# Optimization experiments

Hardware: AMD Instinct MI355X
Metric: run time of the kernel (lower is better)

The kernel has to match this reference:

```python
import jax, jax.numpy as jnp
import numpy as np

T, IN, BATCH = 512, 512, 256
HID, WID = 1024, 512


def setup_inputs() -> dict:
    key = jax.random.key(0)
    k_x, k_wh, k_bh, k_wy, k_by, k_h0 = jax.random.split(key, 6)
    s_h = 1.0 / np.sqrt(HID + IN)  # stabilise sigmoid pre-activations
    s_y = 1.0 / np.sqrt(HID)
    return {
        "xs": jax.random.normal(k_x, (T, IN, BATCH), dtype=jnp.float32),
        "W_h": jax.random.normal(k_wh, (HID, HID + IN), dtype=jnp.float32) * s_h,
        "b_h": jax.random.normal(k_bh, (HID, 1), dtype=jnp.float32) * 0.1,
        "W_y": jax.random.normal(k_wy, (WID, HID), dtype=jnp.float32) * s_y,
        "b_y": jax.random.normal(k_by, (WID, 1), dtype=jnp.float32) * 0.1,
        "h0": jax.random.normal(k_h0, (HID, 1), dtype=jnp.float32),
    }


def reference(xs, W_h, b_h, W_y, b_y, h0):
    # xs: [T, input_size, batch]; returns ys: [T, width, batch]
    batch = xs.shape[2]
    h_init = jnp.tile(h0, (1, batch))  # [HID, batch]

    def step(h, x):
        z = jnp.concatenate([h, x], axis=0)          # [HID+IN, batch]
        h_new = jax.nn.sigmoid(W_h @ z + b_h)        # [HID, batch]
        y = jax.nn.sigmoid(W_y @ h_new + b_y)        # [WID, batch]
        return h_new, y

    _, ys = jax.lax.scan(step, h_init, xs)
    return ys
```

## Files before the change

kernel.cpp:

```cpp
#include <hip/hip_runtime.h>
#include <hip/hip_bf16.h>

#define T_STEPS 512
#define INP     512
#define NB      256
#define HID     1024
#define WID     512
#define KZ      1536
#define ZSZ     (NB * KZ)

typedef short          bf16x8   __attribute__((ext_vector_type(8)));
typedef float          f32x4    __attribute__((ext_vector_type(4)));
typedef float          f32x2    __attribute__((ext_vector_type(2)));
typedef unsigned short ushort8  __attribute__((ext_vector_type(8)));
typedef unsigned short ushort2v __attribute__((ext_vector_type(2)));
typedef unsigned short ushort4v __attribute__((ext_vector_type(4)));
typedef unsigned long long u64;

__device__ __forceinline__ unsigned short f2bf(float x) {
  __hip_bfloat16 h = __float2bfloat16(x);
  return __builtin_bit_cast(unsigned short, h);
}
__device__ __forceinline__ float sigm(float x) { return 1.0f / (1.0f + __expf(-x)); }

#define ZLOAD(dst, p) \
  asm volatile("global_load_dwordx4 %0, %1, off sc0 sc1" : "=v"(dst) : "v"(p))
#define ZWAIT() do { \
  asm volatile("s_waitcnt vmcnt(0)" ::: "memory"); \
  __builtin_amdgcn_sched_barrier(0); \
} while (0)

__device__ __forceinline__ void zst4(unsigned short* p, ushort2v v) {
  __hip_atomic_store((unsigned*)p, __builtin_bit_cast(unsigned, v),
                     __ATOMIC_RELAXED, __HIP_MEMORY_SCOPE_AGENT);
}
__device__ __forceinline__ void zst8(unsigned short* p, ushort4v v) {
  __hip_atomic_store((u64*)p, __builtin_bit_cast(u64, v),
                     __ATOMIC_RELAXED, __HIP_MEMORY_SCOPE_AGENT);
}

__device__ __forceinline__ void poll1(unsigned* p, unsigned tgt) {
  while (__hip_atomic_load(p, __ATOMIC_RELAXED, __HIP_MEMORY_SCOPE_AGENT) < tgt)
    __builtin_amdgcn_s_sleep(1);
}
__device__ __forceinline__ void poll2(u64* p, unsigned lo, unsigned hi) {
  for (;;) {
    const u64 v = __hip_atomic_load(p, __ATOMIC_RELAXED, __HIP_MEMORY_SCOPE_AGENT);
    if ((unsigned)v >= lo && (unsigned)(v >> 32) >= hi) return;
    __builtin_amdgcn_s_sleep(1);
  }
}
__device__ __forceinline__ void arrive(unsigned* ctr) {
  asm volatile("s_waitcnt vmcnt(0)" ::: "memory");
  __syncthreads();
  if (threadIdx.x == 0)
    __hip_atomic_fetch_add(ctr, 1u, __ATOMIC_RELAXED, __HIP_MEMORY_SCOPE_AGENT);
}

__global__ void elman_setup(const float* __restrict__ h0, const float* __restrict__ xs,
                            unsigned short* __restrict__ zT, unsigned* __restrict__ bars) {
  const int b = blockIdx.x;
  if (b == 0) {
    for (int j = threadIdx.x; j < 512; j += blockDim.x) bars[j] = 0u;
  }
  for (int k = threadIdx.x; k < KZ; k += blockDim.x) {
    const float v = (k < HID) ? h0[k] : xs[(size_t)(k - HID) * NB + b];
    zT[(size_t)b * KZ + k] = f2bf(v);
  }
  for (int i = threadIdx.x; i < INP; i += blockDim.x)
    zT[(size_t)ZSZ + (size_t)b * KZ + HID + i] = f2bf(xs[(size_t)(INP + i) * NB + b]);
}

#define PSTR 36
#define PWSZ (32 * PSTR)

__global__ void __launch_bounds__(512, 2) elman_seq(
    const float* __restrict__ xs,
    const float* __restrict__ Wh, const float* __restrict__ bh,
    const float* __restrict__ Wy, const float* __restrict__ by,
    unsigned short* __restrict__ zT, float* __restrict__ out,
    unsigned* __restrict__ bars) {
  __shared__ float P[8 * PWSZ];
  const int wg = blockIdx.x, tid = threadIdx.x;
  const int w = tid >> 6, lane = tid & 63;
  const int lr = lane & 15, lk = lane >> 4;
  unsigned* bar = bars + (wg & 7) * 64;

  if (wg < 128) {
    const int m0 = (wg >> 3) * 64;
    const int n0 = (wg & 7) * 32;
    const int kw = w * 192;
    bf16x8 A[4][6];
#pragma unroll
    for (int mt = 0; mt < 4; ++mt)
#pragma unroll
      for (int kc = 0; kc < 6; ++kc) {
        const float* wp = Wh + (size_t)(m0 + mt * 16 + lr) * KZ + kw + kc * 32 + lk * 8;
        const f32x4 f0 = *(const f32x4*)wp;
        const f32x4 f1 = *(const f32x4*)(wp + 4);
        ushort8 a;
#pragma unroll
        for (int e = 0; e < 4; ++e) { a[e] = f2bf(f0[e]); a[4 + e] = f2bf(f1[e]); }
        A[mt][kc] = __builtin_bit_cast(bf16x8, a);
      }
    const int lcol = tid >> 4;
    const int r2 = (tid & 15) * 2;
    f32x2 bias[2];
#pragma unroll
    for (int hf = 0; hf < 2; ++hf) bias[hf] = *(const f32x2*)&bh[m0 + hf * 32 + r2];
    float* Pw = P + w * PWSZ;

    for (int t = 0; t <= T_STEPS; ++t) {
      if (t < T_STEPS) {
        const unsigned short* zc = zT + (size_t)(t & 3) * ZSZ;
        unsigned short* zn = zT + (size_t)((t + 1) & 3) * ZSZ;
        if (t >= 1) {
          if (tid == 0) poll2((u64*)bar, 16u * (unsigned)t,
                              (t >= 2) ? 8u * (unsigned)(t - 1) : 0u);
          __syncthreads();
        }
        const unsigned short* zb = zc + (size_t)(n0 + lr) * KZ + kw + lk * 8;
        bf16x8 bfr[6][2];
#pragma unroll
        for (int kc = 0; kc < 6; ++kc)
#pragma unroll
          for (int nt = 0; nt < 2; ++nt)
            ZLOAD(bfr[kc][nt], zb + nt * (16 * KZ) + kc * 32);
        ZWAIT();
        f32x4 acc[4][2];
#pragma unroll
        for (int mt = 0; mt < 4; ++mt)
#pragma unroll
          for (int nt = 0; nt < 2; ++nt) acc[mt][nt] = (f32x4){0.f, 0.f, 0.f, 0.f};
#pragma unroll
        for (int kc = 0; kc < 6; ++kc)
#pragma unroll
          for (int nt = 0; nt < 2; ++nt)
#pragma unroll
            for (int mt = 0; mt < 4; ++mt)
              acc[mt][nt] = __builtin_amdgcn_mfma_f32_16x16x32_bf16(A[mt][kc], bfr[kc][nt], acc[mt][nt], 0, 0, 0);
        if (t >= 3 && tid == 0) poll1(bar + 2, 8u * (unsigned)(t - 2));
        __syncthreads();
#pragma unroll
        for (int hf = 0; hf < 2; ++hf) {
#pragma unroll
          for (int mp = 0; mp < 2; ++mp) {
            const int mt = hf * 2 + mp;
#pragma unroll
            for (int nt = 0; nt < 2; ++nt)
              *(f32x4*)&Pw[(nt * 16 + lr) * PSTR + mp * 16 + lk * 4] = acc[mt][nt];
          }
          __syncthreads();
          f32x2 s = {0.f, 0.f};
#pragma unroll
          for (int ww = 0; ww < 8; ++ww)
            s += *(const f32x2*)&P[ww * PWSZ + lcol * PSTR + r2];
          s += bias[hf];
          ushort2v o2;
          o2[0] = f2bf(sigm(s[0]));
          o2[1] = f2bf(sigm(s[1]));
          zst4(zn + (size_t)(n0 + lcol) * KZ + m0 + hf * 32 + r2, o2);
          if (hf == 0) __syncthreads();
        }
      }
      arrive(bar + 0);
    }

  } else if (wg < 192) {
    const int idx = wg - 128;
    const int m0 = (idx >> 3) * 64;
    const int n0 = (idx & 7) * 32;
    const int kw = w * 128;
    bf16x8 A[4][4];
#pragma unroll
    for (int mt = 0; mt < 4; ++mt)
#pragma unroll
      for (int kc = 0; kc < 4; ++kc) {
        const float* wp = Wy + (size_t)(m0 + mt * 16 + lr) * HID + kw + kc * 32 + lk * 8;
        const f32x4 f0 = *(const f32x4*)wp;
        const f32x4 f1 = *(const f32x4*)(wp + 4);
        ushort8 a;
#pragma unroll
        for (int e = 0; e < 4; ++e) { a[e] = f2bf(f0[e]); a[4 + e] = f2bf(f1[e]); }
        A[mt][kc] = __builtin_bit_cast(bf16x8, a);
      }
    const int lcol = tid & 31;
    const int r2 = (tid >> 5) * 2;
    f32x2 bias[2];
#pragma unroll
    for (int hf = 0; hf < 2; ++hf) bias[hf] = *(const f32x2*)&by[m0 + hf * 32 + r2];
    float* Pw = P + w * PWSZ;

    for (int t = 0; t <= T_STEPS; ++t) {
      if (t >= 1) {
        const unsigned short* zc = zT + (size_t)(t & 3) * ZSZ;
        if (tid == 0) poll1(bar + 0, 16u * (unsigned)t);
        __syncthreads();
        const unsigned short* zb = zc + (size_t)(n0 + lr) * KZ + kw + lk * 8;
        bf16x8 bfr[4][2];
#pragma unroll
        for (int kc = 0; kc < 4; ++kc)
#pragma unroll
          for (int nt = 0; nt < 2; ++nt)
            ZLOAD(bfr[kc][nt], zb + nt * (16 * KZ) + kc * 32);
        ZWAIT();
        f32x4 acc[4][2];
#pragma unroll
        for (int mt = 0; mt < 4; ++mt)
#pragma unroll
          for (int nt = 0; nt < 2; ++nt) acc[mt][nt] = (f32x4){0.f, 0.f, 0.f, 0.f};
#pragma unroll
        for (int kc = 0; kc < 4; ++kc)
#pragma unroll
          for (int nt = 0; nt < 2; ++nt)
#pragma unroll
            for (int mt = 0; mt < 4; ++mt)
              acc[mt][nt] = __builtin_amdgcn_mfma_f32_16x16x32_bf16(A[mt][kc], bfr[kc][nt], acc[mt][nt], 0, 0, 0);
        float* op = out + (size_t)(t - 1) * (WID * NB);
        __syncthreads();
#pragma unroll
        for (int hf = 0; hf < 2; ++hf) {
#pragma unroll
          for (int mp = 0; mp < 2; ++mp) {
            const int mt = hf * 2 + mp;
#pragma unroll
            for (int nt = 0; nt < 2; ++nt)
              *(f32x4*)&Pw[(nt * 16 + lr) * PSTR + mp * 16 + lk * 4] = acc[mt][nt];
          }
          __syncthreads();
          f32x2 s = {0.f, 0.f};
#pragma unroll
          for (int ww = 0; ww < 8; ++ww)
            s += *(const f32x2*)&P[ww * PWSZ + lcol * PSTR + r2];
          s += bias[hf];
          const int row = m0 + hf * 32 + r2;
          op[(size_t)(row + 0) * NB + n0 + lcol] = sigm(s[0]);
          op[(size_t)(row + 1) * NB + n0 + lcol] = sigm(s[1]);
          if (hf == 0) __syncthreads();
        }
      }
      arrive(bar + 2);
    }

  } else {
    const int xi = wg - 192;
    const int i0 = (xi >> 3) * 64;
    const int b0 = (xi & 7) * 32;
    const int c = tid & 31, rb = tid >> 5;
    for (int t = 0; t <= T_STEPS; ++t) {
      if (t <= T_STEPS - 3) {
        unsigned short* zx = zT + (size_t)((t + 2) & 3) * ZSZ;
        const float* xp = xs + (size_t)(t + 2) * (INP * NB) + (size_t)(i0 + rb * 4) * NB + b0 + c;
        ushort4v o;
#pragma unroll
        for (int j = 0; j < 4; ++j) o[j] = f2bf(xp[(size_t)j * NB]);
        if (t >= 2) {
          if (tid == 0) poll1(bar + 0, 16u * (unsigned)(t - 1));
        }
        __syncthreads();
        zst8(zx + (size_t)(b0 + c) * KZ + HID + i0 + rb * 4, o);
      }
      arrive(bar + 1);
    }
  }
}

extern "C" void kernel_launch(void* const* d_in, const int* in_sizes, int n_in,
                              void* d_out, int out_size, void* d_ws, size_t ws_size,
                              hipStream_t stream) {
  (void)in_sizes; (void)n_in; (void)out_size; (void)ws_size;
  const float* xs  = (const float*)d_in[0];
  const float* W_h = (const float*)d_in[1];
  const float* b_h = (const float*)d_in[2];
  const float* W_y = (const float*)d_in[3];
  const float* b_y = (const float*)d_in[4];
  const float* h0  = (const float*)d_in[5];
  float* out = (float*)d_out;

  unsigned short* zT = (unsigned short*)d_ws;
  unsigned* bars = (unsigned*)(zT + 4 * (size_t)ZSZ);

  elman_setup<<<dim3(NB), dim3(256), 0, stream>>>(h0, xs, zT, bars);

  void* args[8];
  args[0] = (void*)&xs;  args[1] = (void*)&W_h; args[2] = (void*)&b_h;
  args[3] = (void*)&W_y; args[4] = (void*)&b_y; args[5] = (void*)&zT;
  args[6] = (void*)&out; args[7] = (void*)&bars;
  hipLaunchCooperativeKernel((void*)elman_seq, dim3(256), dim3(512), args, 0u, stream);
}
```

Measured before the change: 3.068 ms.

## Detect same-XCD groups at runtime and use L2-coherent loads/stores instead of system-coherent

At kernel start every workgroup records its XCC id and joins a grid-wide handshake, then checks whether all 32 workgroups sharing its barrier group sit on the same XCD. If they do, the z-buffer loads drop the sc1 bit and the stores become plain stores, relying on the shared L2 for coherence instead of bypassing to memory. A slow path keeps the old fully coherent accesses. The hidden-state poll now reads three counters in one vector load, which replaces the separate mid-step wait on the y-phase counter. The handshake needs all 256 workgroups to be resident at once, and the fast path's correctness depends on the same-XCD check being right.

```diff
diff --git a/kernel.cpp b/kernel.cpp
--- a/kernel.cpp
+++ b/kernel.cpp
@@ -15,6 +15,7 @@
 typedef unsigned short ushort8  __attribute__((ext_vector_type(8)));
 typedef unsigned short ushort2v __attribute__((ext_vector_type(2)));
 typedef unsigned short ushort4v __attribute__((ext_vector_type(4)));
+typedef unsigned       uint4v   __attribute__((ext_vector_type(4)));
 typedef unsigned long long u64;
 
 __device__ __forceinline__ unsigned short f2bf(float x) {
@@ -23,30 +24,38 @@
 }
 __device__ __forceinline__ float sigm(float x) { return 1.0f / (1.0f + __expf(-x)); }
 
-#define ZLOAD(dst, p) \
+#define ZLOAD_FAST(dst, p) \
+  asm volatile("global_load_dwordx4 %0, %1, off sc0" : "=v"(dst) : "v"(p))
+#define ZLOAD_SLOW(dst, p) \
   asm volatile("global_load_dwordx4 %0, %1, off sc0 sc1" : "=v"(dst) : "v"(p))
 #define ZWAIT() do { \
   asm volatile("s_waitcnt vmcnt(0)" ::: "memory"); \
   __builtin_amdgcn_sched_barrier(0); \
 } while (0)
 
+template <bool FAST>
 __device__ __forceinline__ void zst4(unsigned short* p, ushort2v v) {
-  __hip_atomic_store((unsigned*)p, __builtin_bit_cast(unsigned, v),
-                     __ATOMIC_RELAXED, __HIP_MEMORY_SCOPE_AGENT);
-}
+  if constexpr (FAST) *(unsigned*)p = __builtin_bit_cast(unsigned, v);
+  else __hip_atomic_store((unsigned*)p, __builtin_bit_cast(unsigned, v),
+                          __ATOMIC_RELAXED, __HIP_MEMORY_SCOPE_AGENT);
+}
+template <bool FAST>
 __device__ __forceinline__ void zst8(unsigned short* p, ushort4v v) {
-  __hip_atomic_store((u64*)p, __builtin_bit_cast(u64, v),
-                     __ATOMIC_RELAXED, __HIP_MEMORY_SCOPE_AGENT);
+  if constexpr (FAST) *(u64*)p = __builtin_bit_cast(u64, v);
+  else __hip_atomic_store((u64*)p, __builtin_bit_cast(u64, v),
+                          __ATOMIC_RELAXED, __HIP_MEMORY_SCOPE_AGENT);
 }
 
 __device__ __forceinline__ void poll1(unsigned* p, unsigned tgt) {
   while (__hip_atomic_load(p, __ATOMIC_RELAXED, __HIP_MEMORY_SCOPE_AGENT) < tgt)
     __builtin_amdgcn_s_sleep(1);
 }
-__device__ __forceinline__ void poll2(u64* p, unsigned lo, unsigned hi) {
+__device__ __forceinline__ void pollh(unsigned* bar, unsigned ht, unsigned xt, unsigned yt) {
+  uint4v v;
   for (;;) {
-    const u64 v = __hip_atomic_load(p, __ATOMIC_RELAXED, __HIP_MEMORY_SCOPE_AGENT);
-    if ((unsigned)v >= lo && (unsigned)(v >> 32) >= hi) return;
+    asm volatile("global_load_dwordx4 %0, %1, off sc0 sc1\n\ts_waitcnt vmcnt(0)"
+                 : "=v"(v) : "v"(bar) : "memory");
+    if (v.x >= ht && v.y >= xt && v.z >= yt) return;
     __builtin_amdgcn_s_sleep(1);
   }
 }
@@ -61,7 +70,7 @@
                             unsigned short* __restrict__ zT, unsigned* __restrict__ bars) {
   const int b = blockIdx.x;
   if (b == 0) {
-    for (int j = threadIdx.x; j < 512; j += blockDim.x) bars[j] = 0u;
+    for (int j = threadIdx.x; j < 1024; j += blockDim.x) bars[j] = 0u;
   }
   for (int k = threadIdx.x; k < KZ; k += blockDim.x) {
     const float v = (k < HID) ? h0[k] : xs[(size_t)(k - HID) * NB + b];
@@ -74,17 +83,15 @@
 #define PSTR 36
 #define PWSZ (32 * PSTR)
 
-__global__ void __launch_bounds__(512, 2) elman_seq(
+template <bool FAST>
+__device__ __forceinline__ void run_phases(
     const float* __restrict__ xs,
     const float* __restrict__ Wh, const float* __restrict__ bh,
     const float* __restrict__ Wy, const float* __restrict__ by,
     unsigned short* __restrict__ zT, float* __restrict__ out,
-    unsigned* __restrict__ bars) {
-  __shared__ float P[8 * PWSZ];
-  const int wg = blockIdx.x, tid = threadIdx.x;
+    unsigned* bar, float* P, int wg, int tid) {
   const int w = tid >> 6, lane = tid & 63;
   const int lr = lane & 15, lk = lane >> 4;
-  unsigned* bar = bars + (wg & 7) * 64;
 
   if (wg < 128) {
     const int m0 = (wg >> 3) * 64;
@@ -115,8 +122,8 @@
         const unsigned short* zc = zT + (size_t)(t & 3) * ZSZ;
         unsigned short* zn = zT + (size_t)((t + 1) & 3) * ZSZ;
         if (t >= 1) {
-          if (tid == 0) poll2((u64*)bar, 16u * (unsigned)t,
-                              (t >= 2) ? 8u * (unsigned)(t - 1) : 0u);
+          if (tid == 0) pollh(bar, 16u * (unsigned)t, 8u * (unsigned)(t - 1),
+                              (t >= 2) ? 8u * (unsigned)(t - 2) : 0u);
           __syncthreads();
         }
         const unsigned short* zb = zc + (size_t)(n0 + lr) * KZ + kw + lk * 8;
@@ -124,8 +131,10 @@
 #pragma unroll
         for (int kc = 0; kc < 6; ++kc)
 #pragma unroll
-          for (int nt = 0; nt < 2; ++nt)
-            ZLOAD(bfr[kc][nt], zb + nt * (16 * KZ) + kc * 32);
+          for (int nt = 0; nt < 2; ++nt) {
+            if constexpr (FAST) ZLOAD_FAST(bfr[kc][nt], zb + nt * (16 * KZ) + kc * 32);
+            else                ZLOAD_SLOW(bfr[kc][nt], zb + nt * (16 * KZ) + kc * 32);
+          }
         ZWAIT();
         f32x4 acc[4][2];
 #pragma unroll
@@ -139,7 +148,6 @@
 #pragma unroll
             for (int mt = 0; mt < 4; ++mt)
               acc[mt][nt] = __builtin_amdgcn_mfma_f32_16x16x32_bf16(A[mt][kc], bfr[kc][nt], acc[mt][nt], 0, 0, 0);
-        if (t >= 3 && tid == 0) poll1(bar + 2, 8u * (unsigned)(t - 2));
         __syncthreads();
 #pragma unroll
         for (int hf = 0; hf < 2; ++hf) {
@@ -159,7 +167,7 @@
           ushort2v o2;
           o2[0] = f2bf(sigm(s[0]));
           o2[1] = f2bf(sigm(s[1]));
-          zst4(zn + (size_t)(n0 + lcol) * KZ + m0 + hf * 32 + r2, o2);
+          zst4<FAST>(zn + (size_t)(n0 + lcol) * KZ + m0 + hf * 32 + r2, o2);
           if (hf == 0) __syncthreads();
         }
       }
@@ -201,8 +209,10 @@
 #pragma unroll
         for (int kc = 0; kc < 4; ++kc)
 #pragma unroll
-          for (int nt = 0; nt < 2; ++nt)
-            ZLOAD(bfr[kc][nt], zb + nt * (16 * KZ) + kc * 32);
+          for (int nt = 0; nt < 2; ++nt) {
+            if constexpr (FAST) ZLOAD_FAST(bfr[kc][nt], zb + nt * (16 * KZ) + kc * 32);
+            else                ZLOAD_SLOW(bfr[kc][nt], zb + nt * (16 * KZ) + kc * 32);
+          }
         ZWAIT();
         f32x4 acc[4][2];
 #pragma unroll
@@ -258,11 +268,47 @@
           if (tid == 0) poll1(bar + 0, 16u * (unsigned)(t - 1));
         }
         __syncthreads();
-        zst8(zx + (size_t)(b0 + c) * KZ + HID + i0 + rb * 4, o);
+        zst8<FAST>(zx + (size_t)(b0 + c) * KZ + HID + i0 + rb * 4, o);
       }
       arrive(bar + 1);
     }
   }
+}
+
+__global__ void __launch_bounds__(512, 2) elman_seq(
+    const float* __restrict__ xs,
+    const float* __restrict__ Wh, const float* __restrict__ bh,
+    const float* __restrict__ Wy, const float* __restrict__ by,
+    unsigned short* __restrict__ zT, float* __restrict__ out,
+    unsigned* __restrict__ bars) {
+  __shared__ float P[8 * PWSZ];
+  __shared__ unsigned modeSh;
+  const int wg = blockIdx.x, tid = threadIdx.x;
+  unsigned* bar  = bars + (wg & 7) * 64;
+  unsigned* xcds = bars + 512;
+  unsigned* hbar = bars + 768;
+
+  unsigned xcc;
+  asm volatile("s_getreg_b32 %0, hwreg(HW_REG_XCC_ID)" : "=s"(xcc));
+  if (tid == 0) {
+    __hip_atomic_store(&xcds[wg], xcc + 1u, __ATOMIC_RELAXED, __HIP_MEMORY_SCOPE_AGENT);
+    asm volatile("s_waitcnt vmcnt(0)" ::: "memory");
+    __hip_atomic_fetch_add(hbar, 1u, __ATOMIC_RELAXED, __HIP_MEMORY_SCOPE_AGENT);
+    while (__hip_atomic_load(hbar, __ATOMIC_RELAXED, __HIP_MEMORY_SCOPE_AGENT) < 256u)
+      __builtin_amdgcn_s_sleep(1);
+    const unsigned v0 = __hip_atomic_load(&xcds[wg & 7], __ATOMIC_RELAXED, __HIP_MEMORY_SCOPE_AGENT);
+    unsigned m = 1u;
+    for (int j = 1; j < 32; ++j)
+      m &= (__hip_atomic_load(&xcds[(wg & 7) + 8 * j], __ATOMIC_RELAXED,
+                              __HIP_MEMORY_SCOPE_AGENT) == v0) ? 1u : 0u;
+    modeSh = m;
+  }
+  __syncthreads();
+
+  if (modeSh)
+    run_phases<true >(xs, Wh, bh, Wy, by, zT, out, bar, P, wg, tid);
+  else
+    run_phases<false>(xs, Wh, bh, Wy, by, zT, out, bar, P, wg, tid);
 }
 
 extern "C" void kernel_launch(void* const* d_in, const int* in_sizes, int n_in,
```

Result: faster. 2.725 ms (-11.2%).
